# Kernel tuning notes

Measured on AMD Instinct MI355X. Metric: run time of the kernel, lower is better.

The kernel has to match this reference:

```python
import jax, jax.numpy as jnp
import numpy as np

HIDDEN = 128
IN_SIZE = 1
OUT_SIZE = 1
ENC_T = 8192
DEC_T = 4096


def _lstm_step(h, c, x, Wih, Whh, bih, bhh):
    # PyTorch LSTM gate order: i, f, g, o
    gates = Wih @ x + Whh @ h + bih + bhh  # [4H]
    i, f, g, o = jnp.split(gates, 4)
    c = jax.nn.sigmoid(f) * c + jax.nn.sigmoid(i) * jnp.tanh(g)
    h = jax.nn.sigmoid(o) * jnp.tanh(c)
    return h, c


def setup_inputs() -> dict:
    key = jax.random.key(0)
    ks = jax.random.split(key, 12)
    k = 1.0 / np.sqrt(HIDDEN)  # PyTorch default init bound
    u = lambda kk, shape: jax.random.uniform(kk, shape, jnp.float32, -k, k)
    return {
        "input_seq": jax.random.normal(ks[0], (ENC_T,), jnp.float32),
        "enc_Wih": u(ks[1], (4 * HIDDEN, IN_SIZE)),
        "enc_Whh": u(ks[2], (4 * HIDDEN, HIDDEN)),
        "enc_bih": u(ks[3], (4 * HIDDEN,)),
        "enc_bhh": u(ks[4], (4 * HIDDEN,)),
        "dec_Wih": u(ks[5], (4 * HIDDEN, OUT_SIZE)),
        "dec_Whh": u(ks[6], (4 * HIDDEN, HIDDEN)),
        "dec_bih": u(ks[7], (4 * HIDDEN,)),
        "dec_bhh": u(ks[8], (4 * HIDDEN,)),
        "fc_W": u(ks[9], (OUT_SIZE, HIDDEN)),
        "fc_b": u(ks[10], (OUT_SIZE,)),
        "target_seq_len": DEC_T,
    }


def reference(input_seq, enc_Wih, enc_Whh, enc_bih, enc_bhh,
              dec_Wih, dec_Whh, dec_bih, dec_bhh, fc_W, fc_b,
              target_seq_len):
    H = enc_Whh.shape[1]
    dt = input_seq.dtype

    def enc_step(carry, xt):
        h, c = carry
        h, c = _lstm_step(h, c, xt[None], enc_Wih, enc_Whh, enc_bih, enc_bhh)
        return (h, c), None

    (h, c), _ = jax.lax.scan(enc_step,
                             (jnp.zeros(H, dt), jnp.zeros(H, dt)),
                             input_seq)

    def dec_step(carry, _):
        h, c, y = carry  # y: previous prediction, shape [1]
        h, c = _lstm_step(h, c, y, dec_Wih, dec_Whh, dec_bih, dec_bhh)
        pred = fc_W @ h + fc_b  # [1]
        return (h, c, pred), pred

    _, preds = jax.lax.scan(dec_step, (h, c, jnp.zeros(1, dt)),
                            None, length=target_seq_len)
    # preds: [T_out, 1] -> torch.cat(outputs, dim=1) gives [1, T_out]
    return preds.T
```

## Files before the change

### kernel.cpp

```cpp
#include <hip/hip_runtime.h>


#define H      128
#define ENC_T  8192
#define DEC_T  4096
#define NT     512
#define NBLK   256
#define MAGIC  0xC0FFEEu
#define PSLICE 648

__device__ __forceinline__ float sigm(float x) {
    return __builtin_amdgcn_rcpf(1.0f + __expf(-x));
}
__device__ __forceinline__ float tanhfast(float x) {
    return 1.0f - 2.0f * __builtin_amdgcn_rcpf(1.0f + __expf(2.0f * x));
}
__device__ __forceinline__ float rdlane(float v, int l) {
    return __int_as_float(__builtin_amdgcn_readlane(__float_as_int(v), l));
}

__global__ __launch_bounds__(NT, 2)
void seq2seq_lstm(const float* __restrict__ input_seq,
                  const float* __restrict__ enc_Wih,
                  const float* __restrict__ enc_Whh,
                  const float* __restrict__ enc_bih,
                  const float* __restrict__ enc_bhh,
                  const float* __restrict__ dec_Wih,
                  const float* __restrict__ dec_Whh,
                  const float* __restrict__ dec_bih,
                  const float* __restrict__ dec_bhh,
                  const float* __restrict__ fc_W,
                  const float* __restrict__ fc_b,
                  float* __restrict__ out,
                  unsigned* __restrict__ wsflag)
{
    if (blockIdx.x != 0) {
        if (threadIdx.x >= 64) return;
        float z0 = 1.0f, z1 = 1.1f, z2 = 0.9f, z3 = 1.05f;
        for (int it = 0; it < 400000; ++it) {
            unsigned f = 0;
            if (threadIdx.x == 0)
                f = __hip_atomic_load(wsflag, __ATOMIC_RELAXED, __HIP_MEMORY_SCOPE_AGENT);
            f = (unsigned)__shfl((int)f, 0, 64);
            if (f == MAGIC) break;
#pragma unroll
            for (int k = 0; k < 8; ++k) {
                z0 = fmaf(z0, 1.0009765625f, 1e-7f);
                z1 = fmaf(z1, 0.9990234375f, 1e-7f);
                z2 = fmaf(z2, 1.0009765625f, 1e-7f);
                z3 = fmaf(z3, 0.9990234375f, 1e-7f);
            }
            __builtin_amdgcn_s_sleep(4);
        }
        if (z0 + z1 + z2 + z3 == 12345.678f && threadIdx.x == 63)
            wsflag[1] = 7u;
        return;
    }

    __shared__ __align__(16) float xin[ENC_T];
    __shared__ __align__(16) float hbuf[2][H];
    __shared__ __align__(16) float part[2][8 * PSLICE];

    const int t    = threadIdx.x;
    const int lane = t & 63;
    const int wv   = t >> 6;
    const int jb   = 16 * wv;
    const int qq   = lane >> 2;
    const int g    = lane & 3;
    const int myu  = jb + qq;
    const int myrow = g * H + myu;
    const int prd  = 5 * myu + g;
    const int pwb  = wv * PSLICE + 5 * lane;

    {
        const float4* s = (const float4*)input_seq;
        float4* d = (float4*)xin;
        for (int i = t; i < ENC_T / 4; i += NT) d[i] = s[i];
    }

    float4 w4[8][4];
#pragma unroll
    for (int s = 0; s < 8; ++s) {
        const float4* Wr = (const float4*)(enc_Whh + (64 * s + lane) * H + jb);
#pragma unroll
        for (int mq = 0; mq < 4; ++mq) w4[s][mq] = Wr[mq];
    }
    float bias_r = enc_bih[myrow] + enc_bhh[myrow];
    float wih_r  = enc_Wih[myrow];

    float cst = 0.f;
    float hn  = 0.f;
    __syncthreads();

#define MATVEC(PB)                                                          \
    {                                                                       \
        float acc[8];                                                       \
        _Pragma("unroll") for (int s = 0; s < 8; ++s) acc[s] = 0.f;         \
        _Pragma("unroll") for (int mq = 0; mq < 4; ++mq) {                  \
            const float s0 = rdlane(hn, 16 * mq + 3);                       \
            _Pragma("unroll") for (int s = 0; s < 8; ++s)                   \
                acc[s] = fmaf(w4[s][mq].x, s0, acc[s]);                     \
            const float s1 = rdlane(hn, 16 * mq + 7);                       \
            _Pragma("unroll") for (int s = 0; s < 8; ++s)                   \
                acc[s] = fmaf(w4[s][mq].y, s1, acc[s]);                     \
            const float s2 = rdlane(hn, 16 * mq + 11);                      \
            _Pragma("unroll") for (int s = 0; s < 8; ++s)                   \
                acc[s] = fmaf(w4[s][mq].z, s2, acc[s]);                     \
            const float s3 = rdlane(hn, 16 * mq + 15);                      \
            _Pragma("unroll") for (int s = 0; s < 8; ++s)                   \
                acc[s] = fmaf(w4[s][mq].w, s3, acc[s]);                     \
        }                                                                   \
             \
        float* pb_ = &part[PB][pwb];                                        \
        pb_[0]   = acc[0]; pb_[320] = acc[1];                               \
        pb_[1]   = acc[2]; pb_[321] = acc[3];                               \
        pb_[2]   = acc[4]; pb_[322] = acc[5];                               \
        pb_[3]   = acc[6]; pb_[323] = acc[7];                               \
    }

#define REDUCE_UPDATE(PB, ABASE)                                            \
    {                                                                       \
        float a = (ABASE);                                                  \
        _Pragma("unroll") for (int s = 0; s < 8; ++s)                       \
            a += part[PB][s * PSLICE + prd];                                \
        const float v = (g == 2) ? tanhfast(a) : sigm(a);                   \
        const int qb = lane & ~3;                                           \
        const float vi = __shfl(v, qb,     64);                             \
        const float vf = __shfl(v, qb + 1, 64);                             \
        const float vg = __shfl(v, qb + 2, 64);                             \
        const float vo = __shfl(v, qb + 3, 64);                             \
        cst = fmaf(vf, cst, vi * vg);                                       \
        hn  = vo * tanhfast(cst);                                           \
        if (g == 3) hbuf[PB][myu] = hn;                                     \
    }

    for (int st = 0; st < ENC_T; ++st) {
        const int pb = st & 1;
        MATVEC(pb);
        const float x = xin[st];
        __syncthreads();
        REDUCE_UPDATE(pb, fmaf(wih_r, x, bias_r));
    }

    const float fcb = fc_b[0];
    const float fwl = fc_W[lane];
    const float fwh = fc_W[64 + lane];
#pragma unroll
    for (int s = 0; s < 8; ++s) {
        const int r = 64 * s + lane;
        const float vi = dec_Wih[r];
        const float4* Wr = (const float4*)(dec_Whh + r * H + jb);
        const float4* Fr = (const float4*)(fc_W + jb);
#pragma unroll
        for (int mq = 0; mq < 4; ++mq) {
            const float4 dw = Wr[mq], fw = Fr[mq];
            w4[s][mq].x = fmaf(vi, fw.x, dw.x);
            w4[s][mq].y = fmaf(vi, fw.y, dw.y);
            w4[s][mq].z = fmaf(vi, fw.z, dw.z);
            w4[s][mq].w = fmaf(vi, fw.w, dw.w);
        }
    }
    wih_r  = dec_Wih[myrow];
    bias_r = dec_bih[myrow] + dec_bhh[myrow] + wih_r * fcb;
    __syncthreads();
    float q0;
    {
        float p = fmaf(fwl, hbuf[1][lane], fwh * hbuf[1][64 + lane]);
#pragma unroll
        for (int m = 32; m >= 1; m >>= 1) p += __shfl_xor(p, m, 64);
        q0 = p + fcb;
    }
    float cb = bias_r - wih_r * q0;

    for (int st = 0; st < DEC_T; ++st) {
        const int pb = st & 1;
        MATVEC(pb);
        if (wv == 7 && st >= 2) {
            float p = fmaf(fwl, hbuf[pb][lane], fwh * hbuf[pb][64 + lane]);
#pragma unroll
            for (int m = 32; m >= 1; m >>= 1) p += __shfl_xor(p, m, 64);
            if (lane == 0) out[st - 2] = p + fcb;
        }
        __syncthreads();
        REDUCE_UPDATE(pb, cb);
        cb = bias_r;
    }

    __syncthreads();
    if (wv == 7) {
        float p0 = fmaf(fwl, hbuf[0][lane], fwh * hbuf[0][64 + lane]);
        float p1 = fmaf(fwl, hbuf[1][lane], fwh * hbuf[1][64 + lane]);
#pragma unroll
        for (int m = 32; m >= 1; m >>= 1) {
            p0 += __shfl_xor(p0, m, 64);
            p1 += __shfl_xor(p1, m, 64);
        }
        if (lane == 0) {
            out[DEC_T - 2] = p0 + fcb;
            out[DEC_T - 1] = p1 + fcb;
        }
    }
    if (t == 0)
        __hip_atomic_store(wsflag, MAGIC, __ATOMIC_RELEASE, __HIP_MEMORY_SCOPE_AGENT);
}

extern "C" void kernel_launch(void* const* d_in, const int* in_sizes, int n_in,
                              void* d_out, int out_size, void* d_ws, size_t ws_size,
                              hipStream_t stream)
{
    (void)in_sizes; (void)n_in; (void)ws_size; (void)out_size;
    seq2seq_lstm<<<NBLK, NT, 0, stream>>>(
        (const float*)d_in[0],
        (const float*)d_in[1],
        (const float*)d_in[2],
        (const float*)d_in[3],
        (const float*)d_in[4],
        (const float*)d_in[5],
        (const float*)d_in[6],
        (const float*)d_in[7],
        (const float*)d_in[8],
        (const float*)d_in[9],
        (const float*)d_in[10],
        (float*)d_out,
        (unsigned*)d_ws);
}
```

Baseline: 9.126 ms.

## Replace fp32 FMA matvec with split int8 MFMA recurrent matvec

Each LSTM step's recurrent matvec now runs on int8 MFMA instructions. Weights and the hidden state are quantized to 16-bit fixed point and split into high and low bytes, and the products are recombined with three MFMA accumulations per gate. This removes the shared-memory partial-sum reduction and per-wave readlane broadcasts: each lane computes all four gates for its unit, and the packed hidden state is exchanged through a small LDS buffer with one barrier per step. The fc projection also moves onto MFMA. The cost is fixed-point quantization error and extra MFMA latency on a serial dependency chain.

```diff
diff --git a/kernel.cpp b/kernel.cpp
--- a/kernel.cpp
+++ b/kernel.cpp
@@ -7,17 +7,31 @@
 #define NT     512
 #define NBLK   256
 #define MAGIC  0xC0FFEEu
-#define PSLICE 648
-
+
+typedef int v4i __attribute__((ext_vector_type(4)));
+typedef unsigned long long u64;
+
+__device__ __forceinline__ v4i mfma_i8(u64 a, u64 b, v4i c) {
+    return __builtin_amdgcn_mfma_i32_16x16x32_i8((long)a, (long)b, c, 0, 0, 0);
+}
 __device__ __forceinline__ float sigm(float x) {
     return __builtin_amdgcn_rcpf(1.0f + __expf(-x));
 }
 __device__ __forceinline__ float tanhfast(float x) {
     return 1.0f - 2.0f * __builtin_amdgcn_rcpf(1.0f + __expf(2.0f * x));
 }
-__device__ __forceinline__ float rdlane(float v, int l) {
-    return __int_as_float(__builtin_amdgcn_readlane(__float_as_int(v), l));
-}
+template <int C>
+__device__ __forceinline__ int qpermi(int v) {
+    return __builtin_amdgcn_mov_dpp(v, C, 0xf, 0xf, true);
+}
+__device__ __forceinline__ int q16w(float v) {
+    int V = (int)rintf(v * 262144.f);
+    return V > 32639 ? 32639 : (V < -32768 ? -32768 : V);
+}
+
+#define S1 0x1p-17f
+#define S2 0x1p-25f
+#define S3 0x1p-33f
 
 __global__ __launch_bounds__(NT, 2)
 void seq2seq_lstm(const float* __restrict__ input_seq,
@@ -58,147 +72,242 @@
     }
 
     __shared__ __align__(16) float xin[ENC_T];
-    __shared__ __align__(16) float hbuf[2][H];
-    __shared__ __align__(16) float part[2][8 * PSLICE];
+    __shared__ __align__(16) char  hq[2][2][H];
 
     const int t    = threadIdx.x;
     const int lane = t & 63;
     const int wv   = t >> 6;
-    const int jb   = 16 * wv;
-    const int qq   = lane >> 2;
-    const int g    = lane & 3;
-    const int myu  = jb + qq;
-    const int myrow = g * H + myu;
-    const int prd  = 5 * myu + g;
-    const int pwb  = wv * PSLICE + 5 * lane;
+    const int m    = lane & 15;
+    const int grp  = lane >> 4;
+    const int koff = grp * 8;
+    const int myu  = 16 * wv + grp * 4 + (lane & 3);
+    const int ubase = 16 * wv + grp * 4;
+    const bool b0 = (lane & 1), b1 = ((lane >> 1) & 1);
 
     {
         const float4* s = (const float4*)input_seq;
         float4* d = (float4*)xin;
         for (int i = t; i < ENC_T / 4; i += NT) d[i] = s[i];
     }
-
-    float4 w4[8][4];
-#pragma unroll
-    for (int s = 0; s < 8; ++s) {
-        const float4* Wr = (const float4*)(enc_Whh + (64 * s + lane) * H + jb);
-#pragma unroll
-        for (int mq = 0; mq < 4; ++mq) w4[s][mq] = Wr[mq];
-    }
-    float bias_r = enc_bih[myrow] + enc_bhh[myrow];
-    float wih_r  = enc_Wih[myrow];
-
+    if (t < 128) ((int*)hq)[t] = 0;
+
+    u64 whi[4][4], wlo[4][4];
+#pragma unroll
+    for (int g = 0; g < 4; ++g) {
+        const float* Wr = enc_Whh + (g * H + 16 * wv + m) * H;
+#pragma unroll
+        for (int s = 0; s < 4; ++s) {
+            u64 hi = 0, lo = 0;
+#pragma unroll
+            for (int j = 0; j < 8; ++j) {
+                const int V = q16w(Wr[32 * s + koff + j]);
+                const int h8 = (V + 128) >> 8;
+                const int l8 = V - (h8 << 8);
+                hi |= (u64)(h8 & 255) << (8 * j);
+                lo |= (u64)(l8 & 255) << (8 * j);
+            }
+            whi[g][s] = hi; wlo[g][s] = lo;
+        }
+    }
+    float biasv[4], wihv[4];
+#pragma unroll
+    for (int g = 0; g < 4; ++g) {
+        const int r = g * H + myu;
+        biasv[g] = enc_bih[r] + enc_bhh[r];
+        wihv[g]  = enc_Wih[r];
+    }
+
+    const v4i z4 = {0, 0, 0, 0};
     float cst = 0.f;
-    float hn  = 0.f;
     __syncthreads();
-
-#define MATVEC(PB)                                                          \
-    {                                                                       \
-        float acc[8];                                                       \
-        _Pragma("unroll") for (int s = 0; s < 8; ++s) acc[s] = 0.f;         \
-        _Pragma("unroll") for (int mq = 0; mq < 4; ++mq) {                  \
-            const float s0 = rdlane(hn, 16 * mq + 3);                       \
-            _Pragma("unroll") for (int s = 0; s < 8; ++s)                   \
-                acc[s] = fmaf(w4[s][mq].x, s0, acc[s]);                     \
-            const float s1 = rdlane(hn, 16 * mq + 7);                       \
-            _Pragma("unroll") for (int s = 0; s < 8; ++s)                   \
-                acc[s] = fmaf(w4[s][mq].y, s1, acc[s]);                     \
-            const float s2 = rdlane(hn, 16 * mq + 11);                      \
-            _Pragma("unroll") for (int s = 0; s < 8; ++s)                   \
-                acc[s] = fmaf(w4[s][mq].z, s2, acc[s]);                     \
-            const float s3 = rdlane(hn, 16 * mq + 15);                      \
-            _Pragma("unroll") for (int s = 0; s < 8; ++s)                   \
-                acc[s] = fmaf(w4[s][mq].w, s3, acc[s]);                     \
-        }                                                                   \
-             \
-        float* pb_ = &part[PB][pwb];                                        \
-        pb_[0]   = acc[0]; pb_[320] = acc[1];                               \
-        pb_[1]   = acc[2]; pb_[321] = acc[3];                               \
-        pb_[2]   = acc[4]; pb_[322] = acc[5];                               \
-        pb_[3]   = acc[6]; pb_[323] = acc[7];                               \
-    }
-
-#define REDUCE_UPDATE(PB, ABASE)                                            \
-    {                                                                       \
-        float a = (ABASE);                                                  \
-        _Pragma("unroll") for (int s = 0; s < 8; ++s)                       \
-            a += part[PB][s * PSLICE + prd];                                \
-        const float v = (g == 2) ? tanhfast(a) : sigm(a);                   \
-        const int qb = lane & ~3;                                           \
-        const float vi = __shfl(v, qb,     64);                             \
-        const float vf = __shfl(v, qb + 1, 64);                             \
-        const float vg = __shfl(v, qb + 2, 64);                             \
-        const float vo = __shfl(v, qb + 3, 64);                             \
-        cst = fmaf(vf, cst, vi * vg);                                       \
-        hn  = vo * tanhfast(cst);                                           \
-        if (g == 3) hbuf[PB][myu] = hn;                                     \
-    }
 
     for (int st = 0; st < ENC_T; ++st) {
         const int pb = st & 1;
-        MATVEC(pb);
+        u64 bhi[4], blo[4];
+#pragma unroll
+        for (int s = 0; s < 4; ++s) {
+            bhi[s] = *(const u64*)&hq[pb][0][32 * s + koff];
+            blo[s] = *(const u64*)&hq[pb][1][32 * s + koff];
+        }
         const float x = xin[st];
+        v4i d1[4], d2[4], d3[4];
+#pragma unroll
+        for (int g = 0; g < 4; ++g) {
+            v4i a1 = z4, a2 = z4, a3 = z4;
+#pragma unroll
+            for (int s = 0; s < 4; ++s) {
+                a1 = mfma_i8(whi[g][s], bhi[s], a1);
+                a2 = mfma_i8(whi[g][s], blo[s], a2);
+                a2 = mfma_i8(wlo[g][s], bhi[s], a2);
+                a3 = mfma_i8(wlo[g][s], blo[s], a3);
+            }
+            d1[g] = a1; d2[g] = a2; d3[g] = a3;
+        }
+        float gate[4];
+#pragma unroll
+        for (int g = 0; g < 4; ++g) {
+            const int v1 = b1 ? (b0 ? d1[g].w : d1[g].z) : (b0 ? d1[g].y : d1[g].x);
+            const int v2 = b1 ? (b0 ? d2[g].w : d2[g].z) : (b0 ? d2[g].y : d2[g].x);
+            const int v3 = b1 ? (b0 ? d3[g].w : d3[g].z) : (b0 ? d3[g].y : d3[g].x);
+            gate[g] = fmaf((float)v1, S1,
+                      fmaf((float)v2, S2,
+                      fmaf((float)v3, S3, fmaf(wihv[g], x, biasv[g]))));
+        }
+        const float vi = sigm(gate[0]), vf = sigm(gate[1]);
+        const float vg = tanhfast(gate[2]), vo = sigm(gate[3]);
+        cst = fmaf(vf, cst, vi * vg);
+        const float hn = vo * tanhfast(cst);
+
+        int V = (int)rintf(hn * 32768.f);
+        V = V > 32639 ? 32639 : V;
+        const int h8 = (V + 128) >> 8;
+        const int l8 = V - (h8 << 8);
+        const int ph = (h8 & 255) | ((qpermi<0x39>(h8) & 255) << 8)
+                     | ((qpermi<0x4E>(h8) & 255) << 16) | ((qpermi<0x93>(h8) & 255) << 24);
+        const int pl = (l8 & 255) | ((qpermi<0x39>(l8) & 255) << 8)
+                     | ((qpermi<0x4E>(l8) & 255) << 16) | ((qpermi<0x93>(l8) & 255) << 24);
+        if ((lane & 15) == 0) {
+            *(int*)&hq[pb ^ 1][0][ubase] = ph;
+            *(int*)&hq[pb ^ 1][1][ubase] = pl;
+        }
         __syncthreads();
-        REDUCE_UPDATE(pb, fmaf(wih_r, x, bias_r));
     }
 
     const float fcb = fc_b[0];
-    const float fwl = fc_W[lane];
-    const float fwh = fc_W[64 + lane];
-#pragma unroll
-    for (int s = 0; s < 8; ++s) {
-        const int r = 64 * s + lane;
-        const float vi = dec_Wih[r];
-        const float4* Wr = (const float4*)(dec_Whh + r * H + jb);
-        const float4* Fr = (const float4*)(fc_W + jb);
-#pragma unroll
-        for (int mq = 0; mq < 4; ++mq) {
-            const float4 dw = Wr[mq], fw = Fr[mq];
-            w4[s][mq].x = fmaf(vi, fw.x, dw.x);
-            w4[s][mq].y = fmaf(vi, fw.y, dw.y);
-            w4[s][mq].z = fmaf(vi, fw.z, dw.z);
-            w4[s][mq].w = fmaf(vi, fw.w, dw.w);
-        }
-    }
-    wih_r  = dec_Wih[myrow];
-    bias_r = dec_bih[myrow] + dec_bhh[myrow] + wih_r * fcb;
-    __syncthreads();
-    float q0;
+#pragma unroll
+    for (int g = 0; g < 4; ++g) {
+        const int rowbase = g * H + 16 * wv + m;
+        const float* Wr = dec_Whh + rowbase * H;
+        const float vi = dec_Wih[rowbase];
+#pragma unroll
+        for (int s = 0; s < 4; ++s) {
+            u64 hi = 0, lo = 0;
+#pragma unroll
+            for (int j = 0; j < 8; ++j) {
+                const int k = 32 * s + koff + j;
+                const int V = q16w(fmaf(vi, fc_W[k], Wr[k]));
+                const int h8 = (V + 128) >> 8;
+                const int l8 = V - (h8 << 8);
+                hi |= (u64)(h8 & 255) << (8 * j);
+                lo |= (u64)(l8 & 255) << (8 * j);
+            }
+            whi[g][s] = hi; wlo[g][s] = lo;
+        }
+    }
+    u64 fhi[4], flo[4];
+#pragma unroll
+    for (int s = 0; s < 4; ++s) {
+        u64 hi = 0, lo = 0;
+        if (m == 0) {
+#pragma unroll
+            for (int j = 0; j < 8; ++j) {
+                const int V = q16w(fc_W[32 * s + koff + j]);
+                const int h8 = (V + 128) >> 8;
+                const int l8 = V - (h8 << 8);
+                hi |= (u64)(h8 & 255) << (8 * j);
+                lo |= (u64)(l8 & 255) << (8 * j);
+            }
+        }
+        fhi[s] = hi; flo[s] = lo;
+    }
+    float biasD[4], cbv[4];
     {
-        float p = fmaf(fwl, hbuf[1][lane], fwh * hbuf[1][64 + lane]);
-#pragma unroll
-        for (int m = 32; m >= 1; m >>= 1) p += __shfl_xor(p, m, 64);
-        q0 = p + fcb;
-    }
-    float cb = bias_r - wih_r * q0;
+        const int Va = ((int)(signed char)hq[0][0][lane] << 8)
+                     + (int)(signed char)hq[0][1][lane];
+        const int Vb = ((int)(signed char)hq[0][0][64 + lane] << 8)
+                     + (int)(signed char)hq[0][1][64 + lane];
+        float p = fmaf(fc_W[lane], (float)Va * 0x1p-15f,
+                       fc_W[64 + lane] * ((float)Vb * 0x1p-15f));
+#pragma unroll
+        for (int mm = 32; mm >= 1; mm >>= 1) p += __shfl_xor(p, mm, 64);
+        const float q0 = p + fcb;
+#pragma unroll
+        for (int g = 0; g < 4; ++g) {
+            const int r = g * H + myu;
+            const float vi = dec_Wih[r];
+            wihv[g]  = vi;
+            biasD[g] = dec_bih[r] + dec_bhh[r] + vi * fcb;
+            cbv[g]   = biasD[g] - vi * q0;
+        }
+    }
 
     for (int st = 0; st < DEC_T; ++st) {
         const int pb = st & 1;
-        MATVEC(pb);
-        if (wv == 7 && st >= 2) {
-            float p = fmaf(fwl, hbuf[pb][lane], fwh * hbuf[pb][64 + lane]);
-#pragma unroll
-            for (int m = 32; m >= 1; m >>= 1) p += __shfl_xor(p, m, 64);
-            if (lane == 0) out[st - 2] = p + fcb;
+        u64 bhi[4], blo[4];
+#pragma unroll
+        for (int s = 0; s < 4; ++s) {
+            bhi[s] = *(const u64*)&hq[pb][0][32 * s + koff];
+            blo[s] = *(const u64*)&hq[pb][1][32 * s + koff];
+        }
+        v4i d1[4], d2[4], d3[4];
+#pragma unroll
+        for (int g = 0; g < 4; ++g) {
+            v4i a1 = z4, a2 = z4, a3 = z4;
+#pragma unroll
+            for (int s = 0; s < 4; ++s) {
+                a1 = mfma_i8(whi[g][s], bhi[s], a1);
+                a2 = mfma_i8(whi[g][s], blo[s], a2);
+                a2 = mfma_i8(wlo[g][s], bhi[s], a2);
+                a3 = mfma_i8(wlo[g][s], blo[s], a3);
+            }
+            d1[g] = a1; d2[g] = a2; d3[g] = a3;
+        }
+        if (wv == 7) {
+            v4i e1 = z4, e2 = z4, e3 = z4;
+#pragma unroll
+            for (int s = 0; s < 4; ++s) {
+                e1 = mfma_i8(fhi[s], bhi[s], e1);
+                e2 = mfma_i8(fhi[s], blo[s], e2);
+                e2 = mfma_i8(flo[s], bhi[s], e2);
+                e3 = mfma_i8(flo[s], blo[s], e3);
+            }
+            if (lane == 0 && st > 0)
+                out[st - 1] = fmaf((float)e1.x, S1,
+                              fmaf((float)e2.x, S2,
+                              fmaf((float)e3.x, S3, fcb)));
+        }
+        float gate[4];
+#pragma unroll
+        for (int g = 0; g < 4; ++g) {
+            const int v1 = b1 ? (b0 ? d1[g].w : d1[g].z) : (b0 ? d1[g].y : d1[g].x);
+            const int v2 = b1 ? (b0 ? d2[g].w : d2[g].z) : (b0 ? d2[g].y : d2[g].x);
+            const int v3 = b1 ? (b0 ? d3[g].w : d3[g].z) : (b0 ? d3[g].y : d3[g].x);
+            gate[g] = fmaf((float)v1, S1,
+                      fmaf((float)v2, S2,
+                      fmaf((float)v3, S3, cbv[g])));
+        }
+        const float vi = sigm(gate[0]), vf = sigm(gate[1]);
+        const float vg = tanhfast(gate[2]), vo = sigm(gate[3]);
+        cst = fmaf(vf, cst, vi * vg);
+        const float hn = vo * tanhfast(cst);
+
+        int V = (int)rintf(hn * 32768.f);
+        V = V > 32639 ? 32639 : V;
+        const int h8 = (V + 128) >> 8;
+        const int l8 = V - (h8 << 8);
+        const int ph = (h8 & 255) | ((qpermi<0x39>(h8) & 255) << 8)
+                     | ((qpermi<0x4E>(h8) & 255) << 16) | ((qpermi<0x93>(h8) & 255) << 24);
+        const int pl = (l8 & 255) | ((qpermi<0x39>(l8) & 255) << 8)
+                     | ((qpermi<0x4E>(l8) & 255) << 16) | ((qpermi<0x93>(l8) & 255) << 24);
+        if ((lane & 15) == 0) {
+            *(int*)&hq[pb ^ 1][0][ubase] = ph;
+            *(int*)&hq[pb ^ 1][1][ubase] = pl;
         }
         __syncthreads();
-        REDUCE_UPDATE(pb, cb);
-        cb = bias_r;
-    }
-
-    __syncthreads();
-    if (wv == 7) {
-        float p0 = fmaf(fwl, hbuf[0][lane], fwh * hbuf[0][64 + lane]);
-        float p1 = fmaf(fwl, hbuf[1][lane], fwh * hbuf[1][64 + lane]);
-#pragma unroll
-        for (int m = 32; m >= 1; m >>= 1) {
-            p0 += __shfl_xor(p0, m, 64);
-            p1 += __shfl_xor(p1, m, 64);
-        }
-        if (lane == 0) {
-            out[DEC_T - 2] = p0 + fcb;
-            out[DEC_T - 1] = p1 + fcb;
-        }
+#pragma unroll
+        for (int g = 0; g < 4; ++g) cbv[g] = biasD[g];
+    }
+
+    {
+        const int Va = ((int)(signed char)hq[0][0][lane] << 8)
+                     + (int)(signed char)hq[0][1][lane];
+        const int Vb = ((int)(signed char)hq[0][0][64 + lane] << 8)
+                     + (int)(signed char)hq[0][1][64 + lane];
+        float p = fmaf(fc_W[lane], (float)Va * 0x1p-15f,
+                       fc_W[64 + lane] * ((float)Vb * 0x1p-15f));
+#pragma unroll
+        for (int mm = 32; mm >= 1; mm >>= 1) p += __shfl_xor(p, mm, 64);
+        if (t == 0) out[DEC_T - 1] = p + fcb;
     }
     if (t == 0)
         __hip_atomic_store(wsflag, MAGIC, __ATOMIC_RELEASE, __HIP_MEMORY_SCOPE_AGENT);
```

Measured after the change: 15.23 ms. +66.9%, slower.
